# Performance work log

Hardware: AMD Instinct MI355X
Metric: run time of the kernel (lower is better)

The kernel has to match this reference:

```python
import math
import jax, jax.numpy as jnp
import numpy as np

NUM_HEAD = 8
EPS = 1e-5

def _ln(v, w, b):
    m = jnp.mean(v, axis=-1, keepdims=True)
    var = jnp.var(v, axis=-1, keepdims=True)  # biased var, as torch LayerNorm
    return (v - m) * jax.lax.rsqrt(var + EPS) * w + b

def setup_inputs() -> dict:
    key = jax.random.key(0)
    ks = jax.random.split(key, 5)
    B, T, D, L, Hd = 16, 2048, 512, 768, 512
    return {
        "x": jax.random.normal(ks[0], (B, T, D), jnp.float32),
        "xf": jax.random.normal(ks[1], (B, T, L), jnp.float32),
        "norm_w": jnp.ones((D,), jnp.float32),
        "norm_b": jnp.zeros((D,), jnp.float32),
        "tnorm_w": jnp.ones((L,), jnp.float32),
        "tnorm_b": jnp.zeros((L,), jnp.float32),
        "Wq": jax.random.normal(ks[2], (Hd, D), jnp.float32) * (1.0 / math.sqrt(D)),
        "Wk": jax.random.normal(ks[3], (Hd, L), jnp.float32) * (1.0 / math.sqrt(L)),
        "Wv": jax.random.normal(ks[4], (Hd, L), jnp.float32) * (1.0 / math.sqrt(L)),
    }

def reference(x, xf, norm_w, norm_b, tnorm_w, tnorm_b, Wq, Wk, Wv):
    B, T, _ = x.shape
    Hd = Wq.shape[0]
    H = NUM_HEAD
    d = Hd // H
    q = _ln(x, norm_w, norm_b) @ Wq.T                 # B,T,Hd
    xf_n = _ln(xf, tnorm_w, tnorm_b)
    k = xf_n @ Wk.T                                   # B,T,Hd (N == T)
    v = xf_n @ Wv.T                                   # B,T,Hd
    qh = q.reshape(B, T, H, d)
    kh = k.reshape(B, T, H, d)
    vh = v.reshape(B, T, H, d)
    # per-position, per-head dot product gate (no softmax)
    w = jnp.einsum('bthd,bthd->bth', qh, kh) / math.sqrt(d)
    # dropout in eval mode = identity
    y2 = (w[..., None] * vh).reshape(B, T, Hd)
    y1 = ((1.0 - w)[..., None] * qh).reshape(B, T, Hd)
    return (y1, y2)
```

## Files before the change

kernel.cpp:

```cpp
#include <hip/hip_runtime.h>

#define NT 512
#define MT 64

typedef __attribute__((ext_vector_type(8))) short short8;
typedef __attribute__((ext_vector_type(4))) float f32x4;
typedef __attribute__((ext_vector_type(4))) unsigned short u16x4;

__device__ __forceinline__ unsigned short f2bf(float f) {
  unsigned int u = __builtin_bit_cast(unsigned int, f);
  u += 0x7fffu + ((u >> 16) & 1u);
  return (unsigned short)(u >> 16);
}

__global__ void cvt_weights(const float* __restrict__ wq,
                            const float* __restrict__ wk,
                            const float* __restrict__ wv,
                            unsigned short* __restrict__ o) {
  int stride = gridDim.x * blockDim.x;
  int i0 = blockIdx.x * blockDim.x + threadIdx.x;
  for (int t = i0; t < 32768; t += stride) {
    int lane = t & 63, n = (t >> 6) & 3, kk32 = (t >> 8) & 15, head = t >> 12;
    int row = head * 64 + n * 16 + (lane & 15);
    int k   = kk32 * 32 + (lane >> 4) * 8;
    const float* s = wq + (size_t)row * 512 + k;
    unsigned short* d = o + (size_t)t * 8;
    #pragma unroll
    for (int e = 0; e < 8; ++e) d[e] = f2bf(s[e]);
  }
  for (int t = i0; t < 49152; t += stride) {
    int lane = t & 63, n = (t >> 6) & 3, rem = t >> 8;
    int kk32 = rem % 24, head = rem / 24;
    int row = head * 64 + n * 16 + (lane & 15);
    int k   = kk32 * 32 + (lane >> 4) * 8;
    const float* s = wk + (size_t)row * 768 + k;
    unsigned short* d = o + 262144 + (size_t)t * 8;
    #pragma unroll
    for (int e = 0; e < 8; ++e) d[e] = f2bf(s[e]);
  }
  for (int t = i0; t < 49152; t += stride) {
    int lane = t & 63, n = (t >> 6) & 3, rem = t >> 8;
    int kk32 = rem % 24, head = rem / 24;
    int row = head * 64 + n * 16 + (lane & 15);
    int k   = kk32 * 32 + (lane >> 4) * 8;
    const float* s = wv + (size_t)row * 768 + k;
    unsigned short* d = o + 655360 + (size_t)t * 8;
    #pragma unroll
    for (int e = 0; e < 8; ++e) d[e] = f2bf(s[e]);
  }
}

__global__ __launch_bounds__(NT, 2)
void fused_xattn(const float* __restrict__ x, const float* __restrict__ xf,
                 const float* __restrict__ nw, const float* __restrict__ nb,
                 const float* __restrict__ tw, const float* __restrict__ tb,
                 const unsigned short* __restrict__ wbf,
                 float* __restrict__ out) {
  __shared__ __attribute__((aligned(16))) char smem[98304];
  const int tid   = threadIdx.x;
  const int lane  = tid & 63;
  const int wid   = tid >> 6;
  const int lr    = lane & 15;
  const int lkb   = (lane >> 4) * 8;
  const int lrow4 = (lane >> 4) * 4;

  const long row0 = (long)blockIdx.x * MT;
  float* __restrict__ y1 = out;
  float* __restrict__ y2 = out + 16777216L;

  {
    f32x4 t0[8], t1[8];
    #pragma unroll
    for (int j = 0; j < 8; ++j) {
      const f32x4* rp = (const f32x4*)(x + (row0 + wid + 8 * j) * 512);
      t0[j] = rp[lane]; t1[j] = rp[lane + 64];
    }
    const f32x4* g4 = (const f32x4*)nw;
    const f32x4* b4 = (const f32x4*)nb;
    f32x4 g0 = g4[lane], g1 = g4[lane + 64];
    f32x4 c0 = b4[lane], c1 = b4[lane + 64];
    #pragma unroll
    for (int j = 0; j < 8; ++j) {
      f32x4 a = t0[j], b = t1[j];
      float s  = a.x + a.y + a.z + a.w + b.x + b.y + b.z + b.w;
      float s2 = a.x*a.x + a.y*a.y + a.z*a.z + a.w*a.w
               + b.x*b.x + b.y*b.y + b.z*b.z + b.w*b.w;
      #pragma unroll
      for (int m = 1; m < 64; m <<= 1) { s += __shfl_xor(s, m, 64); s2 += __shfl_xor(s2, m, 64); }
      float mean = s * (1.0f / 512.0f);
      float var  = s2 * (1.0f / 512.0f) - mean * mean;
      float rs   = rsqrtf(var + 1e-5f);
      u16x4 o0 = { f2bf((a.x - mean) * rs * g0.x + c0.x),
                   f2bf((a.y - mean) * rs * g0.y + c0.y),
                   f2bf((a.z - mean) * rs * g0.z + c0.z),
                   f2bf((a.w - mean) * rs * g0.w + c0.w) };
      u16x4 o1 = { f2bf((b.x - mean) * rs * g1.x + c1.x),
                   f2bf((b.y - mean) * rs * g1.y + c1.y),
                   f2bf((b.z - mean) * rs * g1.z + c1.z),
                   f2bf((b.w - mean) * rs * g1.w + c1.w) };
      int r = wid + 8 * j;
      int base = r * 1024, sw = (r & 7) << 4;
      *(u16x4*)(smem + ((base +       lane * 8) ^ sw)) = o0;
      *(u16x4*)(smem + ((base + 512 + lane * 8) ^ sw)) = o1;
    }
  }
  __syncthreads();

  f32x4 fr0[8], fr1[8], fr2[8];
  #pragma unroll
  for (int j = 0; j < 8; ++j) {
    const f32x4* rp = (const f32x4*)(xf + (row0 + wid + 8 * j) * 768);
    fr0[j] = rp[lane]; fr1[j] = rp[lane + 64]; fr2[j] = rp[lane + 128];
  }

  f32x4 qa[4][4] = {};
  {
    const unsigned short* bq = wbf + wid * 32768 + lane * 8;
    short8 bc[4], ac[4];
    #pragma unroll
    for (int n = 0; n < 4; ++n) bc[n] = *(const short8*)(bq + n * 512);
    #pragma unroll
    for (int m = 0; m < 4; ++m) {
      int row = m * 16 + lr;
      ac[m] = *(const short8*)(smem + ((row * 1024 + lkb * 2) ^ ((row & 7) << 4)));
    }
    for (int kk = 0; kk < 16; ++kk) {
      short8 bn[4], an[4];
      if (kk < 15) {
        #pragma unroll
        for (int n = 0; n < 4; ++n)
          bn[n] = *(const short8*)(bq + (kk + 1) * 2048 + n * 512);
        #pragma unroll
        for (int m = 0; m < 4; ++m) {
          int row = m * 16 + lr;
          an[m] = *(const short8*)(smem + ((row * 1024 + ((kk + 1) * 32 + lkb) * 2) ^ ((row & 7) << 4)));
        }
      }
      #pragma unroll
      for (int n = 0; n < 4; ++n)
        #pragma unroll
        for (int m = 0; m < 4; ++m)
          qa[m][n] = __builtin_amdgcn_mfma_f32_16x16x32_bf16(ac[m], bc[n], qa[m][n], 0, 0, 0);
      if (kk < 15) {
        #pragma unroll
        for (int n = 0; n < 4; ++n) bc[n] = bn[n];
        #pragma unroll
        for (int m = 0; m < 4; ++m) ac[m] = an[m];
      }
    }
  }
  __syncthreads();

  {
    const f32x4* g4 = (const f32x4*)tw;
    const f32x4* b4 = (const f32x4*)tb;
    f32x4 g0 = g4[lane], g1 = g4[lane + 64], g2 = g4[lane + 128];
    f32x4 c0 = b4[lane], c1 = b4[lane + 64], c2 = b4[lane + 128];
    #pragma unroll
    for (int j = 0; j < 8; ++j) {
      f32x4 a = fr0[j], b = fr1[j], c = fr2[j];
      float s  = a.x + a.y + a.z + a.w + b.x + b.y + b.z + b.w
               + c.x + c.y + c.z + c.w;
      float s2 = a.x*a.x + a.y*a.y + a.z*a.z + a.w*a.w
               + b.x*b.x + b.y*b.y + b.z*b.z + b.w*b.w
               + c.x*c.x + c.y*c.y + c.z*c.z + c.w*c.w;
      #pragma unroll
      for (int m = 1; m < 64; m <<= 1) { s += __shfl_xor(s, m, 64); s2 += __shfl_xor(s2, m, 64); }
      float mean = s * (1.0f / 768.0f);
      float var  = s2 * (1.0f / 768.0f) - mean * mean;
      float rs   = rsqrtf(var + 1e-5f);
      u16x4 o0 = { f2bf((a.x - mean) * rs * g0.x + c0.x),
                   f2bf((a.y - mean) * rs * g0.y + c0.y),
                   f2bf((a.z - mean) * rs * g0.z + c0.z),
                   f2bf((a.w - mean) * rs * g0.w + c0.w) };
      u16x4 o1 = { f2bf((b.x - mean) * rs * g1.x + c1.x),
                   f2bf((b.y - mean) * rs * g1.y + c1.y),
                   f2bf((b.z - mean) * rs * g1.z + c1.z),
                   f2bf((b.w - mean) * rs * g1.w + c1.w) };
      u16x4 o2 = { f2bf((c.x - mean) * rs * g2.x + c2.x),
                   f2bf((c.y - mean) * rs * g2.y + c2.y),
                   f2bf((c.z - mean) * rs * g2.z + c2.z),
                   f2bf((c.w - mean) * rs * g2.w + c2.w) };
      int r = wid + 8 * j;
      int base = r * 1536, sw = (r & 7) << 4;
      *(u16x4*)(smem + ((base +        lane * 8) ^ sw)) = o0;
      *(u16x4*)(smem + ((base + 512  + lane * 8) ^ sw)) = o1;
      *(u16x4*)(smem + ((base + 1024 + lane * 8) ^ sw)) = o2;
    }
  }
  __syncthreads();

  f32x4 ka[4][4] = {};
  {
    const unsigned short* bk = wbf + 262144 + wid * 49152 + lane * 8;
    short8 bc[4], ac[4];
    #pragma unroll
    for (int n = 0; n < 4; ++n) bc[n] = *(const short8*)(bk + n * 512);
    #pragma unroll
    for (int m = 0; m < 4; ++m) {
      int row = m * 16 + lr;
      ac[m] = *(const short8*)(smem + ((row * 1536 + lkb * 2) ^ ((row & 7) << 4)));
    }
    for (int kk = 0; kk < 24; ++kk) {
      short8 bn[4], an[4];
      if (kk < 23) {
        #pragma unroll
        for (int n = 0; n < 4; ++n)
          bn[n] = *(const short8*)(bk + (kk + 1) * 2048 + n * 512);
        #pragma unroll
        for (int m = 0; m < 4; ++m) {
          int row = m * 16 + lr;
          an[m] = *(const short8*)(smem + ((row * 1536 + ((kk + 1) * 32 + lkb) * 2) ^ ((row & 7) << 4)));
        }
      }
      #pragma unroll
      for (int n = 0; n < 4; ++n)
        #pragma unroll
        for (int m = 0; m < 4; ++m)
          ka[m][n] = __builtin_amdgcn_mfma_f32_16x16x32_bf16(ac[m], bc[n], ka[m][n], 0, 0, 0);
      if (kk < 23) {
        #pragma unroll
        for (int n = 0; n < 4; ++n) bc[n] = bn[n];
        #pragma unroll
        for (int m = 0; m < 4; ++m) ac[m] = an[m];
      }
    }
  }

  float wgt[4][4];
  #pragma unroll
  for (int m = 0; m < 4; ++m) {
    #pragma unroll
    for (int r = 0; r < 4; ++r) {
      float p = 0.0f;
      #pragma unroll
      for (int n = 0; n < 4; ++n) p += qa[m][n][r] * ka[m][n][r];
      #pragma unroll
      for (int msk = 1; msk < 16; msk <<= 1) p += __shfl_xor(p, msk, 64);
      wgt[m][r] = p * 0.125f;
    }
  }
  #pragma unroll
  for (int m = 0; m < 4; ++m) {
    #pragma unroll
    for (int r = 0; r < 4; ++r) {
      float f = 1.0f - wgt[m][r];
      long grow = row0 + m * 16 + lrow4 + r;
      #pragma unroll
      for (int n = 0; n < 4; ++n) {
        int ch = wid * 64 + n * 16 + lr;
        y1[grow * 512 + ch] = f * qa[m][n][r];
      }
    }
  }

  f32x4 va[4][4] = {};
  {
    const unsigned short* bv = wbf + 655360 + wid * 49152 + lane * 8;
    short8 bc[4], ac[4];
    #pragma unroll
    for (int n = 0; n < 4; ++n) bc[n] = *(const short8*)(bv + n * 512);
    #pragma unroll
    for (int m = 0; m < 4; ++m) {
      int row = m * 16 + lr;
      ac[m] = *(const short8*)(smem + ((row * 1536 + lkb * 2) ^ ((row & 7) << 4)));
    }
    for (int kk = 0; kk < 24; ++kk) {
      short8 bn[4], an[4];
      if (kk < 23) {
        #pragma unroll
        for (int n = 0; n < 4; ++n)
          bn[n] = *(const short8*)(bv + (kk + 1) * 2048 + n * 512);
        #pragma unroll
        for (int m = 0; m < 4; ++m) {
          int row = m * 16 + lr;
          an[m] = *(const short8*)(smem + ((row * 1536 + ((kk + 1) * 32 + lkb) * 2) ^ ((row & 7) << 4)));
        }
      }
      #pragma unroll
      for (int n = 0; n < 4; ++n)
        #pragma unroll
        for (int m = 0; m < 4; ++m)
          va[m][n] = __builtin_amdgcn_mfma_f32_16x16x32_bf16(ac[m], bc[n], va[m][n], 0, 0, 0);
      if (kk < 23) {
        #pragma unroll
        for (int n = 0; n < 4; ++n) bc[n] = bn[n];
        #pragma unroll
        for (int m = 0; m < 4; ++m) ac[m] = an[m];
      }
    }
  }
  #pragma unroll
  for (int m = 0; m < 4; ++m) {
    #pragma unroll
    for (int r = 0; r < 4; ++r) {
      float f = wgt[m][r];
      long grow = row0 + m * 16 + lrow4 + r;
      #pragma unroll
      for (int n = 0; n < 4; ++n) {
        int ch = wid * 64 + n * 16 + lr;
        y2[grow * 512 + ch] = f * va[m][n][r];
      }
    }
  }
}

extern "C" void kernel_launch(void* const* d_in, const int* in_sizes, int n_in,
                              void* d_out, int out_size, void* d_ws, size_t ws_size,
                              hipStream_t stream) {
  const float* x  = (const float*)d_in[0];
  const float* xf = (const float*)d_in[1];
  const float* nw = (const float*)d_in[2];
  const float* nb = (const float*)d_in[3];
  const float* tw = (const float*)d_in[4];
  const float* tb = (const float*)d_in[5];
  const float* wq = (const float*)d_in[6];
  const float* wk = (const float*)d_in[7];
  const float* wv = (const float*)d_in[8];
  unsigned short* wbf = (unsigned short*)d_ws;

  cvt_weights<<<256, 256, 0, stream>>>(wq, wk, wv, wbf);
  fused_xattn<<<512, NT, 0, stream>>>(x, xf, nw, nb, tw, tb, wbf, (float*)d_out);
}
```

Baseline: 117.2 us.

## Halve row tile, double grid, and reorder LN/GEMM stages with separate smem buffers

```diff
diff --git a/kernel.cpp b/kernel.cpp
--- a/kernel.cpp
+++ b/kernel.cpp
@@ -1,7 +1,7 @@
 #include <hip/hip_runtime.h>
 
 #define NT 512
-#define MT 64
+#define MT 32
 
 typedef __attribute__((ext_vector_type(8))) short short8;
 typedef __attribute__((ext_vector_type(4))) float f32x4;
@@ -50,13 +50,15 @@
   }
 }
 
-__global__ __launch_bounds__(NT, 2)
+__global__ __launch_bounds__(NT, 4)
 void fused_xattn(const float* __restrict__ x, const float* __restrict__ xf,
                  const float* __restrict__ nw, const float* __restrict__ nb,
                  const float* __restrict__ tw, const float* __restrict__ tb,
                  const unsigned short* __restrict__ wbf,
                  float* __restrict__ out) {
-  __shared__ __attribute__((aligned(16))) char smem[98304];
+  __shared__ __attribute__((aligned(16))) char smem[81920];
+  char* bufA = smem;
+  char* bufB = smem + 49152;
   const int tid   = threadIdx.x;
   const int lane  = tid & 63;
   const int wid   = tid >> 6;
@@ -69,96 +71,19 @@
   float* __restrict__ y2 = out + 16777216L;
 
   {
-    f32x4 t0[8], t1[8];
-    #pragma unroll
-    for (int j = 0; j < 8; ++j) {
-      const f32x4* rp = (const f32x4*)(x + (row0 + wid + 8 * j) * 512);
-      t0[j] = rp[lane]; t1[j] = rp[lane + 64];
-    }
-    const f32x4* g4 = (const f32x4*)nw;
-    const f32x4* b4 = (const f32x4*)nb;
-    f32x4 g0 = g4[lane], g1 = g4[lane + 64];
-    f32x4 c0 = b4[lane], c1 = b4[lane + 64];
-    #pragma unroll
-    for (int j = 0; j < 8; ++j) {
-      f32x4 a = t0[j], b = t1[j];
-      float s  = a.x + a.y + a.z + a.w + b.x + b.y + b.z + b.w;
-      float s2 = a.x*a.x + a.y*a.y + a.z*a.z + a.w*a.w
-               + b.x*b.x + b.y*b.y + b.z*b.z + b.w*b.w;
-      #pragma unroll
-      for (int m = 1; m < 64; m <<= 1) { s += __shfl_xor(s, m, 64); s2 += __shfl_xor(s2, m, 64); }
-      float mean = s * (1.0f / 512.0f);
-      float var  = s2 * (1.0f / 512.0f) - mean * mean;
-      float rs   = rsqrtf(var + 1e-5f);
-      u16x4 o0 = { f2bf((a.x - mean) * rs * g0.x + c0.x),
-                   f2bf((a.y - mean) * rs * g0.y + c0.y),
-                   f2bf((a.z - mean) * rs * g0.z + c0.z),
-                   f2bf((a.w - mean) * rs * g0.w + c0.w) };
-      u16x4 o1 = { f2bf((b.x - mean) * rs * g1.x + c1.x),
-                   f2bf((b.y - mean) * rs * g1.y + c1.y),
-                   f2bf((b.z - mean) * rs * g1.z + c1.z),
-                   f2bf((b.w - mean) * rs * g1.w + c1.w) };
-      int r = wid + 8 * j;
-      int base = r * 1024, sw = (r & 7) << 4;
-      *(u16x4*)(smem + ((base +       lane * 8) ^ sw)) = o0;
-      *(u16x4*)(smem + ((base + 512 + lane * 8) ^ sw)) = o1;
-    }
-  }
-  __syncthreads();
-
-  f32x4 fr0[8], fr1[8], fr2[8];
-  #pragma unroll
-  for (int j = 0; j < 8; ++j) {
-    const f32x4* rp = (const f32x4*)(xf + (row0 + wid + 8 * j) * 768);
-    fr0[j] = rp[lane]; fr1[j] = rp[lane + 64]; fr2[j] = rp[lane + 128];
-  }
-
-  f32x4 qa[4][4] = {};
-  {
-    const unsigned short* bq = wbf + wid * 32768 + lane * 8;
-    short8 bc[4], ac[4];
-    #pragma unroll
-    for (int n = 0; n < 4; ++n) bc[n] = *(const short8*)(bq + n * 512);
-    #pragma unroll
-    for (int m = 0; m < 4; ++m) {
-      int row = m * 16 + lr;
-      ac[m] = *(const short8*)(smem + ((row * 1024 + lkb * 2) ^ ((row & 7) << 4)));
-    }
-    for (int kk = 0; kk < 16; ++kk) {
-      short8 bn[4], an[4];
-      if (kk < 15) {
-        #pragma unroll
-        for (int n = 0; n < 4; ++n)
-          bn[n] = *(const short8*)(bq + (kk + 1) * 2048 + n * 512);
-        #pragma unroll
-        for (int m = 0; m < 4; ++m) {
-          int row = m * 16 + lr;
-          an[m] = *(const short8*)(smem + ((row * 1024 + ((kk + 1) * 32 + lkb) * 2) ^ ((row & 7) << 4)));
-        }
-      }
-      #pragma unroll
-      for (int n = 0; n < 4; ++n)
-        #pragma unroll
-        for (int m = 0; m < 4; ++m)
-          qa[m][n] = __builtin_amdgcn_mfma_f32_16x16x32_bf16(ac[m], bc[n], qa[m][n], 0, 0, 0);
-      if (kk < 15) {
-        #pragma unroll
-        for (int n = 0; n < 4; ++n) bc[n] = bn[n];
-        #pragma unroll
-        for (int m = 0; m < 4; ++m) ac[m] = an[m];
-      }
-    }
-  }
-  __syncthreads();
-
-  {
+    f32x4 t0[4], t1[4], t2[4];
+    #pragma unroll
+    for (int j = 0; j < 4; ++j) {
+      const f32x4* rp = (const f32x4*)(xf + (row0 + wid * 4 + j) * 768);
+      t0[j] = rp[lane]; t1[j] = rp[lane + 64]; t2[j] = rp[lane + 128];
+    }
     const f32x4* g4 = (const f32x4*)tw;
     const f32x4* b4 = (const f32x4*)tb;
     f32x4 g0 = g4[lane], g1 = g4[lane + 64], g2 = g4[lane + 128];
     f32x4 c0 = b4[lane], c1 = b4[lane + 64], c2 = b4[lane + 128];
     #pragma unroll
-    for (int j = 0; j < 8; ++j) {
-      f32x4 a = fr0[j], b = fr1[j], c = fr2[j];
+    for (int j = 0; j < 4; ++j) {
+      f32x4 a = t0[j], b = t1[j], c = t2[j];
       float s  = a.x + a.y + a.z + a.w + b.x + b.y + b.z + b.w
                + c.x + c.y + c.z + c.w;
       float s2 = a.x*a.x + a.y*a.y + a.z*a.z + a.w*a.w
@@ -181,55 +106,131 @@
                    f2bf((c.y - mean) * rs * g2.y + c2.y),
                    f2bf((c.z - mean) * rs * g2.z + c2.z),
                    f2bf((c.w - mean) * rs * g2.w + c2.w) };
-      int r = wid + 8 * j;
+      int r = wid * 4 + j;
       int base = r * 1536, sw = (r & 7) << 4;
-      *(u16x4*)(smem + ((base +        lane * 8) ^ sw)) = o0;
-      *(u16x4*)(smem + ((base + 512  + lane * 8) ^ sw)) = o1;
-      *(u16x4*)(smem + ((base + 1024 + lane * 8) ^ sw)) = o2;
-    }
+      *(u16x4*)(bufA + ((base +        lane * 8) ^ sw)) = o0;
+      *(u16x4*)(bufA + ((base + 512  + lane * 8) ^ sw)) = o1;
+      *(u16x4*)(bufA + ((base + 1024 + lane * 8) ^ sw)) = o2;
+    }
+  }
+
+  f32x4 xr0[4], xr1[4];
+  #pragma unroll
+  for (int j = 0; j < 4; ++j) {
+    const f32x4* rp = (const f32x4*)(x + (row0 + wid * 4 + j) * 512);
+    xr0[j] = rp[lane]; xr1[j] = rp[lane + 64];
   }
   __syncthreads();
 
-  f32x4 ka[4][4] = {};
+  f32x4 ka[2][4] = {};
   {
     const unsigned short* bk = wbf + 262144 + wid * 49152 + lane * 8;
-    short8 bc[4], ac[4];
+    short8 bc[4], ac[2];
     #pragma unroll
     for (int n = 0; n < 4; ++n) bc[n] = *(const short8*)(bk + n * 512);
     #pragma unroll
-    for (int m = 0; m < 4; ++m) {
+    for (int m = 0; m < 2; ++m) {
       int row = m * 16 + lr;
-      ac[m] = *(const short8*)(smem + ((row * 1536 + lkb * 2) ^ ((row & 7) << 4)));
+      ac[m] = *(const short8*)(bufA + ((row * 1536 + lkb * 2) ^ ((row & 7) << 4)));
     }
     for (int kk = 0; kk < 24; ++kk) {
-      short8 bn[4], an[4];
+      short8 bn[4], an[2];
       if (kk < 23) {
         #pragma unroll
         for (int n = 0; n < 4; ++n)
           bn[n] = *(const short8*)(bk + (kk + 1) * 2048 + n * 512);
         #pragma unroll
-        for (int m = 0; m < 4; ++m) {
+        for (int m = 0; m < 2; ++m) {
           int row = m * 16 + lr;
-          an[m] = *(const short8*)(smem + ((row * 1536 + ((kk + 1) * 32 + lkb) * 2) ^ ((row & 7) << 4)));
+          an[m] = *(const short8*)(bufA + ((row * 1536 + ((kk + 1) * 32 + lkb) * 2) ^ ((row & 7) << 4)));
         }
       }
       #pragma unroll
       for (int n = 0; n < 4; ++n)
         #pragma unroll
-        for (int m = 0; m < 4; ++m)
+        for (int m = 0; m < 2; ++m)
           ka[m][n] = __builtin_amdgcn_mfma_f32_16x16x32_bf16(ac[m], bc[n], ka[m][n], 0, 0, 0);
       if (kk < 23) {
         #pragma unroll
         for (int n = 0; n < 4; ++n) bc[n] = bn[n];
         #pragma unroll
-        for (int m = 0; m < 4; ++m) ac[m] = an[m];
-      }
-    }
-  }
-
-  float wgt[4][4];
+        for (int m = 0; m < 2; ++m) ac[m] = an[m];
+      }
+    }
+  }
+
+  {
+    const f32x4* g4 = (const f32x4*)nw;
+    const f32x4* b4 = (const f32x4*)nb;
+    f32x4 g0 = g4[lane], g1 = g4[lane + 64];
+    f32x4 c0 = b4[lane], c1 = b4[lane + 64];
+    #pragma unroll
+    for (int j = 0; j < 4; ++j) {
+      f32x4 a = xr0[j], b = xr1[j];
+      float s  = a.x + a.y + a.z + a.w + b.x + b.y + b.z + b.w;
+      float s2 = a.x*a.x + a.y*a.y + a.z*a.z + a.w*a.w
+               + b.x*b.x + b.y*b.y + b.z*b.z + b.w*b.w;
+      #pragma unroll
+      for (int m = 1; m < 64; m <<= 1) { s += __shfl_xor(s, m, 64); s2 += __shfl_xor(s2, m, 64); }
+      float mean = s * (1.0f / 512.0f);
+      float var  = s2 * (1.0f / 512.0f) - mean * mean;
+      float rs   = rsqrtf(var + 1e-5f);
+      u16x4 o0 = { f2bf((a.x - mean) * rs * g0.x + c0.x),
+                   f2bf((a.y - mean) * rs * g0.y + c0.y),
+                   f2bf((a.z - mean) * rs * g0.z + c0.z),
+                   f2bf((a.w - mean) * rs * g0.w + c0.w) };
+      u16x4 o1 = { f2bf((b.x - mean) * rs * g1.x + c1.x),
+                   f2bf((b.y - mean) * rs * g1.y + c1.y),
+                   f2bf((b.z - mean) * rs * g1.z + c1.z),
+                   f2bf((b.w - mean) * rs * g1.w + c1.w) };
+      int r = wid * 4 + j;
+      int base = r * 1024, sw = (r & 7) << 4;
+      *(u16x4*)(bufB + ((base +       lane * 8) ^ sw)) = o0;
+      *(u16x4*)(bufB + ((base + 512 + lane * 8) ^ sw)) = o1;
+    }
+  }
+  __syncthreads();
+
+  f32x4 qa[2][4] = {};
+  {
+    const unsigned short* bq = wbf + wid * 32768 + lane * 8;
+    short8 bc[4], ac[2];
+    #pragma unroll
+    for (int n = 0; n < 4; ++n) bc[n] = *(const short8*)(bq + n * 512);
+    #pragma unroll
+    for (int m = 0; m < 2; ++m) {
+      int row = m * 16 + lr;
+      ac[m] = *(const short8*)(bufB + ((row * 1024 + lkb * 2) ^ ((row & 7) << 4)));
+    }
+    for (int kk = 0; kk < 16; ++kk) {
+      short8 bn[4], an[2];
+      if (kk < 15) {
+        #pragma unroll
+        for (int n = 0; n < 4; ++n)
+          bn[n] = *(const short8*)(bq + (kk + 1) * 2048 + n * 512);
+        #pragma unroll
+        for (int m = 0; m < 2; ++m) {
+          int row = m * 16 + lr;
+          an[m] = *(const short8*)(bufB + ((row * 1024 + ((kk + 1) * 32 + lkb) * 2) ^ ((row & 7) << 4)));
+        }
+      }
+      #pragma unroll
+      for (int n = 0; n < 4; ++n)
+        #pragma unroll
+        for (int m = 0; m < 2; ++m)
+          qa[m][n] = __builtin_amdgcn_mfma_f32_16x16x32_bf16(ac[m], bc[n], qa[m][n], 0, 0, 0);
+      if (kk < 15) {
+        #pragma unroll
+        for (int n = 0; n < 4; ++n) bc[n] = bn[n];
+        #pragma unroll
+        for (int m = 0; m < 2; ++m) ac[m] = an[m];
+      }
+    }
+  }
+
+  float wgt[2][4];
   #pragma unroll
-  for (int m = 0; m < 4; ++m) {
+  for (int m = 0; m < 2; ++m) {
     #pragma unroll
     for (int r = 0; r < 4; ++r) {
       float p = 0.0f;
@@ -241,7 +242,7 @@
     }
   }
   #pragma unroll
-  for (int m = 0; m < 4; ++m) {
+  for (int m = 0; m < 2; ++m) {
     #pragma unroll
     for (int r = 0; r < 4; ++r) {
       float f = 1.0f - wgt[m][r];
@@ -254,44 +255,44 @@
     }
   }
 
-  f32x4 va[4][4] = {};
+  f32x4 va[2][4] = {};
   {
     const unsigned short* bv = wbf + 655360 + wid * 49152 + lane * 8;
-    short8 bc[4], ac[4];
+    short8 bc[4], ac[2];
     #pragma unroll
     for (int n = 0; n < 4; ++n) bc[n] = *(const short8*)(bv + n * 512);
     #pragma unroll
-    for (int m = 0; m < 4; ++m) {
+    for (int m = 0; m < 2; ++m) {
       int row = m * 16 + lr;
-      ac[m] = *(const short8*)(smem + ((row * 1536 + lkb * 2) ^ ((row & 7) << 4)));
+      ac[m] = *(const short8*)(bufA + ((row * 1536 + lkb * 2) ^ ((row & 7) << 4)));
     }
     for (int kk = 0; kk < 24; ++kk) {
-      short8 bn[4], an[4];
+      short8 bn[4], an[2];
       if (kk < 23) {
         #pragma unroll
         for (int n = 0; n < 4; ++n)
           bn[n] = *(const short8*)(bv + (kk + 1) * 2048 + n * 512);
         #pragma unroll
-        for (int m = 0; m < 4; ++m) {
+        for (int m = 0; m < 2; ++m) {
           int row = m * 16 + lr;
-          an[m] = *(const short8*)(smem + ((row * 1536 + ((kk + 1) * 32 + lkb) * 2) ^ ((row & 7) << 4)));
+          an[m] = *(const short8*)(bufA + ((row * 1536 + ((kk + 1) * 32 + lkb) * 2) ^ ((row & 7) << 4)));
         }
       }
       #pragma unroll
       for (int n = 0; n < 4; ++n)
         #pragma unroll
-        for (int m = 0; m < 4; ++m)
+        for (int m = 0; m < 2; ++m)
           va[m][n] = __builtin_amdgcn_mfma_f32_16x16x32_bf16(ac[m], bc[n], va[m][n], 0, 0, 0);
       if (kk < 23) {
         #pragma unroll
         for (int n = 0; n < 4; ++n) bc[n] = bn[n];
         #pragma unroll
-        for (int m = 0; m < 4; ++m) ac[m] = an[m];
+        for (int m = 0; m < 2; ++m) ac[m] = an[m];
       }
     }
   }
   #pragma unroll
-  for (int m = 0; m < 4; ++m) {
+  for (int m = 0; m < 2; ++m) {
     #pragma unroll
     for (int r = 0; r < 4; ++r) {
       float f = wgt[m][r];
@@ -320,5 +321,5 @@
   unsigned short* wbf = (unsigned short*)d_ws;
 
   cvt_weights<<<256, 256, 0, stream>>>(wq, wk, wv, wbf);
-  fused_xattn<<<512, NT, 0, stream>>>(x, xf, nw, nb, tw, tb, wbf, (float*)d_out);
+  fused_xattn<<<1024, NT, 0, stream>>>(x, xf, nw, nb, tw, tb, wbf, (float*)d_out);
 }
```

After: 196.3 us. 67.4% more time.

## Process two row tiles per block and prefetch next xf tile during GEMMs

Applied to the files above, without the earlier changes.

```diff
diff --git a/kernel.cpp b/kernel.cpp
--- a/kernel.cpp
+++ b/kernel.cpp
@@ -1,7 +1,6 @@
 #include <hip/hip_runtime.h>
 
 #define NT 512
-#define MT 64
 
 typedef __attribute__((ext_vector_type(8))) short short8;
 typedef __attribute__((ext_vector_type(4))) float f32x4;
@@ -56,7 +55,8 @@
                  const float* __restrict__ tw, const float* __restrict__ tb,
                  const unsigned short* __restrict__ wbf,
                  float* __restrict__ out) {
-  __shared__ __attribute__((aligned(16))) char smem[98304];
+  __shared__ __attribute__((aligned(16))) char ldsF[98304];
+  __shared__ __attribute__((aligned(16))) char ldsX[65536];
   const int tid   = threadIdx.x;
   const int lane  = tid & 63;
   const int wid   = tid >> 6;
@@ -64,244 +64,271 @@
   const int lkb   = (lane >> 4) * 8;
   const int lrow4 = (lane >> 4) * 4;
 
-  const long row0 = (long)blockIdx.x * MT;
   float* __restrict__ y1 = out;
   float* __restrict__ y2 = out + 16777216L;
 
+  f32x4 fr0[8], fr1[8], fr2[8];
   {
-    f32x4 t0[8], t1[8];
+    const long r0 = (long)blockIdx.x * 128;
+    #pragma unroll
+    for (int j = 0; j < 8; ++j) {
+      const f32x4* rp = (const f32x4*)(xf + (r0 + wid + 8 * j) * 768);
+      fr0[j] = rp[lane]; fr1[j] = rp[lane + 64]; fr2[j] = rp[lane + 128];
+    }
+  }
+
+  #pragma unroll
+  for (int t = 0; t < 2; ++t) {
+    const long row0 = (long)blockIdx.x * 128 + t * 64;
+
+    {
+      const f32x4* g4 = (const f32x4*)tw;
+      const f32x4* b4 = (const f32x4*)tb;
+      f32x4 g0 = g4[lane], g1 = g4[lane + 64], g2 = g4[lane + 128];
+      f32x4 c0 = b4[lane], c1 = b4[lane + 64], c2 = b4[lane + 128];
+      #pragma unroll
+      for (int j = 0; j < 8; ++j) {
+        f32x4 a = fr0[j], b = fr1[j], c = fr2[j];
+        float s  = a.x + a.y + a.z + a.w + b.x + b.y + b.z + b.w
+                 + c.x + c.y + c.z + c.w;
+        float s2 = a.x*a.x + a.y*a.y + a.z*a.z + a.w*a.w
+                 + b.x*b.x + b.y*b.y + b.z*b.z + b.w*b.w
+                 + c.x*c.x + c.y*c.y + c.z*c.z + c.w*c.w;
+        #pragma unroll
+        for (int m = 1; m < 64; m <<= 1) { s += __shfl_xor(s, m, 64); s2 += __shfl_xor(s2, m, 64); }
+        float mean = s * (1.0f / 768.0f);
+        float var  = s2 * (1.0f / 768.0f) - mean * mean;
+        float rs   = rsqrtf(var + 1e-5f);
+        u16x4 o0 = { f2bf((a.x - mean) * rs * g0.x + c0.x),
+                     f2bf((a.y - mean) * rs * g0.y + c0.y),
+                     f2bf((a.z - mean) * rs * g0.z + c0.z),
+                     f2bf((a.w - mean) * rs * g0.w + c0.w) };
+        u16x4 o1 = { f2bf((b.x - mean) * rs * g1.x + c1.x),
+                     f2bf((b.y - mean) * rs * g1.y + c1.y),
+                     f2bf((b.z - mean) * rs * g1.z + c1.z),
+                     f2bf((b.w - mean) * rs * g1.w + c1.w) };
+        u16x4 o2 = { f2bf((c.x - mean) * rs * g2.x + c2.x),
+                     f2bf((c.y - mean) * rs * g2.y + c2.y),
+                     f2bf((c.z - mean) * rs * g2.z + c2.z),
+                     f2bf((c.w - mean) * rs * g2.w + c2.w) };
+        int r = wid + 8 * j;
+        int base = r * 1536, sw = (r & 7) << 4;
+        *(u16x4*)(ldsF + ((base +        lane * 8) ^ sw)) = o0;
+        *(u16x4*)(ldsF + ((base + 512  + lane * 8) ^ sw)) = o1;
+        *(u16x4*)(ldsF + ((base + 1024 + lane * 8) ^ sw)) = o2;
+      }
+    }
+    __syncthreads();
+
+    f32x4 xr0[8], xr1[8];
     #pragma unroll
     for (int j = 0; j < 8; ++j) {
       const f32x4* rp = (const f32x4*)(x + (row0 + wid + 8 * j) * 512);
-      t0[j] = rp[lane]; t1[j] = rp[lane + 64];
-    }
-    const f32x4* g4 = (const f32x4*)nw;
-    const f32x4* b4 = (const f32x4*)nb;
-    f32x4 g0 = g4[lane], g1 = g4[lane + 64];
-    f32x4 c0 = b4[lane], c1 = b4[lane + 64];
-    #pragma unroll
-    for (int j = 0; j < 8; ++j) {
-      f32x4 a = t0[j], b = t1[j];
-      float s  = a.x + a.y + a.z + a.w + b.x + b.y + b.z + b.w;
-      float s2 = a.x*a.x + a.y*a.y + a.z*a.z + a.w*a.w
-               + b.x*b.x + b.y*b.y + b.z*b.z + b.w*b.w;
-      #pragma unroll
-      for (int m = 1; m < 64; m <<= 1) { s += __shfl_xor(s, m, 64); s2 += __shfl_xor(s2, m, 64); }
-      float mean = s * (1.0f / 512.0f);
-      float var  = s2 * (1.0f / 512.0f) - mean * mean;
-      float rs   = rsqrtf(var + 1e-5f);
-      u16x4 o0 = { f2bf((a.x - mean) * rs * g0.x + c0.x),
-                   f2bf((a.y - mean) * rs * g0.y + c0.y),
-                   f2bf((a.z - mean) * rs * g0.z + c0.z),
-                   f2bf((a.w - mean) * rs * g0.w + c0.w) };
-      u16x4 o1 = { f2bf((b.x - mean) * rs * g1.x + c1.x),
-                   f2bf((b.y - mean) * rs * g1.y + c1.y),
-                   f2bf((b.z - mean) * rs * g1.z + c1.z),
-                   f2bf((b.w - mean) * rs * g1.w + c1.w) };
-      int r = wid + 8 * j;
-      int base = r * 1024, sw = (r & 7) << 4;
-      *(u16x4*)(smem + ((base +       lane * 8) ^ sw)) = o0;
-      *(u16x4*)(smem + ((base + 512 + lane * 8) ^ sw)) = o1;
-    }
-  }
-  __syncthreads();
-
-  f32x4 fr0[8], fr1[8], fr2[8];
-  #pragma unroll
-  for (int j = 0; j < 8; ++j) {
-    const f32x4* rp = (const f32x4*)(xf + (row0 + wid + 8 * j) * 768);
-    fr0[j] = rp[lane]; fr1[j] = rp[lane + 64]; fr2[j] = rp[lane + 128];
-  }
-
-  f32x4 qa[4][4] = {};
-  {
-    const unsigned short* bq = wbf + wid * 32768 + lane * 8;
-    short8 bc[4], ac[4];
-    #pragma unroll
-    for (int n = 0; n < 4; ++n) bc[n] = *(const short8*)(bq + n * 512);
+      xr0[j] = rp[lane]; xr1[j] = rp[lane + 64];
+    }
+
+    f32x4 ka[4][4] = {};
+    {
+      const unsigned short* bk = wbf + 262144 + wid * 49152 + lane * 8;
+      short8 bc[4], ac[4];
+      #pragma unroll
+      for (int n = 0; n < 4; ++n) bc[n] = *(const short8*)(bk + n * 512);
+      #pragma unroll
+      for (int m = 0; m < 4; ++m) {
+        int row = m * 16 + lr;
+        ac[m] = *(const short8*)(ldsF + ((row * 1536 + lkb * 2) ^ ((row & 7) << 4)));
+      }
+      for (int kk = 0; kk < 24; ++kk) {
+        short8 bn[4], an[4];
+        if (kk < 23) {
+          #pragma unroll
+          for (int n = 0; n < 4; ++n)
+            bn[n] = *(const short8*)(bk + (kk + 1) * 2048 + n * 512);
+          #pragma unroll
+          for (int m = 0; m < 4; ++m) {
+            int row = m * 16 + lr;
+            an[m] = *(const short8*)(ldsF + ((row * 1536 + ((kk + 1) * 32 + lkb) * 2) ^ ((row & 7) << 4)));
+          }
+        }
+        #pragma unroll
+        for (int n = 0; n < 4; ++n)
+          #pragma unroll
+          for (int m = 0; m < 4; ++m)
+            ka[m][n] = __builtin_amdgcn_mfma_f32_16x16x32_bf16(ac[m], bc[n], ka[m][n], 0, 0, 0);
+        if (kk < 23) {
+          #pragma unroll
+          for (int n = 0; n < 4; ++n) bc[n] = bn[n];
+          #pragma unroll
+          for (int m = 0; m < 4; ++m) ac[m] = an[m];
+        }
+      }
+    }
+
+    {
+      const f32x4* g4 = (const f32x4*)nw;
+      const f32x4* b4 = (const f32x4*)nb;
+      f32x4 g0 = g4[lane], g1 = g4[lane + 64];
+      f32x4 c0 = b4[lane], c1 = b4[lane + 64];
+      #pragma unroll
+      for (int j = 0; j < 8; ++j) {
+        f32x4 a = xr0[j], b = xr1[j];
+        float s  = a.x + a.y + a.z + a.w + b.x + b.y + b.z + b.w;
+        float s2 = a.x*a.x + a.y*a.y + a.z*a.z + a.w*a.w
+                 + b.x*b.x + b.y*b.y + b.z*b.z + b.w*b.w;
+        #pragma unroll
+        for (int m = 1; m < 64; m <<= 1) { s += __shfl_xor(s, m, 64); s2 += __shfl_xor(s2, m, 64); }
+        float mean = s * (1.0f / 512.0f);
+        float var  = s2 * (1.0f / 512.0f) - mean * mean;
+        float rs   = rsqrtf(var + 1e-5f);
+        u16x4 o0 = { f2bf((a.x - mean) * rs * g0.x + c0.x),
+                     f2bf((a.y - mean) * rs * g0.y + c0.y),
+                     f2bf((a.z - mean) * rs * g0.z + c0.z),
+                     f2bf((a.w - mean) * rs * g0.w + c0.w) };
+        u16x4 o1 = { f2bf((b.x - mean) * rs * g1.x + c1.x),
+                     f2bf((b.y - mean) * rs * g1.y + c1.y),
+                     f2bf((b.z - mean) * rs * g1.z + c1.z),
+                     f2bf((b.w - mean) * rs * g1.w + c1.w) };
+        int r = wid + 8 * j;
+        int base = r * 1024, sw = (r & 7) << 4;
+        *(u16x4*)(ldsX + ((base +       lane * 8) ^ sw)) = o0;
+        *(u16x4*)(ldsX + ((base + 512 + lane * 8) ^ sw)) = o1;
+      }
+    }
+    __syncthreads();
+
+    f32x4 qa[4][4] = {};
+    {
+      const unsigned short* bq = wbf + wid * 32768 + lane * 8;
+      short8 bc[4], ac[4];
+      #pragma unroll
+      for (int n = 0; n < 4; ++n) bc[n] = *(const short8*)(bq + n * 512);
+      #pragma unroll
+      for (int m = 0; m < 4; ++m) {
+        int row = m * 16 + lr;
+        ac[m] = *(const short8*)(ldsX + ((row * 1024 + lkb * 2) ^ ((row & 7) << 4)));
+      }
+      for (int kk = 0; kk < 16; ++kk) {
+        short8 bn[4], an[4];
+        if (kk < 15) {
+          #pragma unroll
+          for (int n = 0; n < 4; ++n)
+            bn[n] = *(const short8*)(bq + (kk + 1) * 2048 + n * 512);
+          #pragma unroll
+          for (int m = 0; m < 4; ++m) {
+            int row = m * 16 + lr;
+            an[m] = *(const short8*)(ldsX + ((row * 1024 + ((kk + 1) * 32 + lkb) * 2) ^ ((row & 7) << 4)));
+          }
+        }
+        #pragma unroll
+        for (int n = 0; n < 4; ++n)
+          #pragma unroll
+          for (int m = 0; m < 4; ++m)
+            qa[m][n] = __builtin_amdgcn_mfma_f32_16x16x32_bf16(ac[m], bc[n], qa[m][n], 0, 0, 0);
+        if (kk < 15) {
+          #pragma unroll
+          for (int n = 0; n < 4; ++n) bc[n] = bn[n];
+          #pragma unroll
+          for (int m = 0; m < 4; ++m) ac[m] = an[m];
+        }
+      }
+    }
+
+    float wgt[4][4];
     #pragma unroll
     for (int m = 0; m < 4; ++m) {
-      int row = m * 16 + lr;
-      ac[m] = *(const short8*)(smem + ((row * 1024 + lkb * 2) ^ ((row & 7) << 4)));
-    }
-    for (int kk = 0; kk < 16; ++kk) {
-      short8 bn[4], an[4];
-      if (kk < 15) {
+      #pragma unroll
+      for (int r = 0; r < 4; ++r) {
+        float p = 0.0f;
+        #pragma unroll
+        for (int n = 0; n < 4; ++n) p += qa[m][n][r] * ka[m][n][r];
+        #pragma unroll
+        for (int msk = 1; msk < 16; msk <<= 1) p += __shfl_xor(p, msk, 64);
+        wgt[m][r] = p * 0.125f;
+      }
+    }
+    #pragma unroll
+    for (int m = 0; m < 4; ++m) {
+      #pragma unroll
+      for (int r = 0; r < 4; ++r) {
+        float f = 1.0f - wgt[m][r];
+        long grow = row0 + m * 16 + lrow4 + r;
+        #pragma unroll
+        for (int n = 0; n < 4; ++n) {
+          int ch = wid * 64 + n * 16 + lr;
+          y1[grow * 512 + ch] = f * qa[m][n][r];
+        }
+      }
+    }
+
+    if (t == 0) {
+      const long r1 = (long)blockIdx.x * 128 + 64;
+      #pragma unroll
+      for (int j = 0; j < 6; ++j) {
+        const f32x4* rp = (const f32x4*)(xf + (r1 + wid + 8 * j) * 768);
+        fr0[j] = rp[lane]; fr1[j] = rp[lane + 64]; fr2[j] = rp[lane + 128];
+      }
+    }
+
+    f32x4 va[4][4] = {};
+    {
+      const unsigned short* bv = wbf + 655360 + wid * 49152 + lane * 8;
+      short8 bc[4], ac[4];
+      #pragma unroll
+      for (int n = 0; n < 4; ++n) bc[n] = *(const short8*)(bv + n * 512);
+      #pragma unroll
+      for (int m = 0; m < 4; ++m) {
+        int row = m * 16 + lr;
+        ac[m] = *(const short8*)(ldsF + ((row * 1536 + lkb * 2) ^ ((row & 7) << 4)));
+      }
+      for (int kk = 0; kk < 24; ++kk) {
+        short8 bn[4], an[4];
+        if (kk < 23) {
+          #pragma unroll
+          for (int n = 0; n < 4; ++n)
+            bn[n] = *(const short8*)(bv + (kk + 1) * 2048 + n * 512);
+          #pragma unroll
+          for (int m = 0; m < 4; ++m) {
+            int row = m * 16 + lr;
+            an[m] = *(const short8*)(ldsF + ((row * 1536 + ((kk + 1) * 32 + lkb) * 2) ^ ((row & 7) << 4)));
+          }
+        }
         #pragma unroll
         for (int n = 0; n < 4; ++n)
-          bn[n] = *(const short8*)(bq + (kk + 1) * 2048 + n * 512);
-        #pragma unroll
-        for (int m = 0; m < 4; ++m) {
-          int row = m * 16 + lr;
-          an[m] = *(const short8*)(smem + ((row * 1024 + ((kk + 1) * 32 + lkb) * 2) ^ ((row & 7) << 4)));
-        }
-      }
-      #pragma unroll
-      for (int n = 0; n < 4; ++n)
-        #pragma unroll
-        for (int m = 0; m < 4; ++m)
-          qa[m][n] = __builtin_amdgcn_mfma_f32_16x16x32_bf16(ac[m], bc[n], qa[m][n], 0, 0, 0);
-      if (kk < 15) {
-        #pragma unroll
-        for (int n = 0; n < 4; ++n) bc[n] = bn[n];
-        #pragma unroll
-        for (int m = 0; m < 4; ++m) ac[m] = an[m];
-      }
-    }
-  }
-  __syncthreads();
-
-  {
-    const f32x4* g4 = (const f32x4*)tw;
-    const f32x4* b4 = (const f32x4*)tb;
-    f32x4 g0 = g4[lane], g1 = g4[lane + 64], g2 = g4[lane + 128];
-    f32x4 c0 = b4[lane], c1 = b4[lane + 64], c2 = b4[lane + 128];
-    #pragma unroll
-    for (int j = 0; j < 8; ++j) {
-      f32x4 a = fr0[j], b = fr1[j], c = fr2[j];
-      float s  = a.x + a.y + a.z + a.w + b.x + b.y + b.z + b.w
-               + c.x + c.y + c.z + c.w;
-      float s2 = a.x*a.x + a.y*a.y + a.z*a.z + a.w*a.w
-               + b.x*b.x + b.y*b.y + b.z*b.z + b.w*b.w
-               + c.x*c.x + c.y*c.y + c.z*c.z + c.w*c.w;
-      #pragma unroll
-      for (int m = 1; m < 64; m <<= 1) { s += __shfl_xor(s, m, 64); s2 += __shfl_xor(s2, m, 64); }
-      float mean = s * (1.0f / 768.0f);
-      float var  = s2 * (1.0f / 768.0f) - mean * mean;
-      float rs   = rsqrtf(var + 1e-5f);
-      u16x4 o0 = { f2bf((a.x - mean) * rs * g0.x + c0.x),
-                   f2bf((a.y - mean) * rs * g0.y + c0.y),
-                   f2bf((a.z - mean) * rs * g0.z + c0.z),
-                   f2bf((a.w - mean) * rs * g0.w + c0.w) };
-      u16x4 o1 = { f2bf((b.x - mean) * rs * g1.x + c1.x),
-                   f2bf((b.y - mean) * rs * g1.y + c1.y),
-                   f2bf((b.z - mean) * rs * g1.z + c1.z),
-                   f2bf((b.w - mean) * rs * g1.w + c1.w) };
-      u16x4 o2 = { f2bf((c.x - mean) * rs * g2.x + c2.x),
-                   f2bf((c.y - mean) * rs * g2.y + c2.y),
-                   f2bf((c.z - mean) * rs * g2.z + c2.z),
-                   f2bf((c.w - mean) * rs * g2.w + c2.w) };
-      int r = wid + 8 * j;
-      int base = r * 1536, sw = (r & 7) << 4;
-      *(u16x4*)(smem + ((base +        lane * 8) ^ sw)) = o0;
-      *(u16x4*)(smem + ((base + 512  + lane * 8) ^ sw)) = o1;
-      *(u16x4*)(smem + ((base + 1024 + lane * 8) ^ sw)) = o2;
-    }
-  }
-  __syncthreads();
-
-  f32x4 ka[4][4] = {};
-  {
-    const unsigned short* bk = wbf + 262144 + wid * 49152 + lane * 8;
-    short8 bc[4], ac[4];
-    #pragma unroll
-    for (int n = 0; n < 4; ++n) bc[n] = *(const short8*)(bk + n * 512);
+          #pragma unroll
+          for (int m = 0; m < 4; ++m)
+            va[m][n] = __builtin_amdgcn_mfma_f32_16x16x32_bf16(ac[m], bc[n], va[m][n], 0, 0, 0);
+        if (kk < 23) {
+          #pragma unroll
+          for (int n = 0; n < 4; ++n) bc[n] = bn[n];
+          #pragma unroll
+          for (int m = 0; m < 4; ++m) ac[m] = an[m];
+        }
+      }
+    }
+
+    if (t == 0) {
+      const long r1 = (long)blockIdx.x * 128 + 64;
+      #pragma unroll
+      for (int j = 6; j < 8; ++j) {
+        const f32x4* rp = (const f32x4*)(xf + (r1 + wid + 8 * j) * 768);
+        fr0[j] = rp[lane]; fr1[j] = rp[lane + 64]; fr2[j] = rp[lane + 128];
+      }
+    }
+
     #pragma unroll
     for (int m = 0; m < 4; ++m) {
-      int row = m * 16 + lr;
-      ac[m] = *(const short8*)(smem + ((row * 1536 + lkb * 2) ^ ((row & 7) << 4)));
-    }
-    for (int kk = 0; kk < 24; ++kk) {
-      short8 bn[4], an[4];
-      if (kk < 23) {
-        #pragma unroll
-        for (int n = 0; n < 4; ++n)
-          bn[n] = *(const short8*)(bk + (kk + 1) * 2048 + n * 512);
-        #pragma unroll
-        for (int m = 0; m < 4; ++m) {
-          int row = m * 16 + lr;
-          an[m] = *(const short8*)(smem + ((row * 1536 + ((kk + 1) * 32 + lkb) * 2) ^ ((row & 7) << 4)));
-        }
-      }
-      #pragma unroll
-      for (int n = 0; n < 4; ++n)
-        #pragma unroll
-        for (int m = 0; m < 4; ++m)
-          ka[m][n] = __builtin_amdgcn_mfma_f32_16x16x32_bf16(ac[m], bc[n], ka[m][n], 0, 0, 0);
-      if (kk < 23) {
-        #pragma unroll
-        for (int n = 0; n < 4; ++n) bc[n] = bn[n];
-        #pragma unroll
-        for (int m = 0; m < 4; ++m) ac[m] = an[m];
-      }
-    }
-  }
-
-  float wgt[4][4];
-  #pragma unroll
-  for (int m = 0; m < 4; ++m) {
-    #pragma unroll
-    for (int r = 0; r < 4; ++r) {
-      float p = 0.0f;
-      #pragma unroll
-      for (int n = 0; n < 4; ++n) p += qa[m][n][r] * ka[m][n][r];
-      #pragma unroll
-      for (int msk = 1; msk < 16; msk <<= 1) p += __shfl_xor(p, msk, 64);
-      wgt[m][r] = p * 0.125f;
-    }
-  }
-  #pragma unroll
-  for (int m = 0; m < 4; ++m) {
-    #pragma unroll
-    for (int r = 0; r < 4; ++r) {
-      float f = 1.0f - wgt[m][r];
-      long grow = row0 + m * 16 + lrow4 + r;
-      #pragma unroll
-      for (int n = 0; n < 4; ++n) {
-        int ch = wid * 64 + n * 16 + lr;
-        y1[grow * 512 + ch] = f * qa[m][n][r];
-      }
-    }
-  }
-
-  f32x4 va[4][4] = {};
-  {
-    const unsigned short* bv = wbf + 655360 + wid * 49152 + lane * 8;
-    short8 bc[4], ac[4];
-    #pragma unroll
-    for (int n = 0; n < 4; ++n) bc[n] = *(const short8*)(bv + n * 512);
-    #pragma unroll
-    for (int m = 0; m < 4; ++m) {
-      int row = m * 16 + lr;
-      ac[m] = *(const short8*)(smem + ((row * 1536 + lkb * 2) ^ ((row & 7) << 4)));
-    }
-    for (int kk = 0; kk < 24; ++kk) {
-      short8 bn[4], an[4];
-      if (kk < 23) {
-        #pragma unroll
-        for (int n = 0; n < 4; ++n)
-          bn[n] = *(const short8*)(bv + (kk + 1) * 2048 + n * 512);
-        #pragma unroll
-        for (int m = 0; m < 4; ++m) {
-          int row = m * 16 + lr;
-          an[m] = *(const short8*)(smem + ((row * 1536 + ((kk + 1) * 32 + lkb) * 2) ^ ((row & 7) << 4)));
-        }
-      }
-      #pragma unroll
-      for (int n = 0; n < 4; ++n)
-        #pragma unroll
-        for (int m = 0; m < 4; ++m)
-          va[m][n] = __builtin_amdgcn_mfma_f32_16x16x32_bf16(ac[m], bc[n], va[m][n], 0, 0, 0);
-      if (kk < 23) {
-        #pragma unroll
-        for (int n = 0; n < 4; ++n) bc[n] = bn[n];
-        #pragma unroll
-        for (int m = 0; m < 4; ++m) ac[m] = an[m];
-      }
-    }
-  }
-  #pragma unroll
-  for (int m = 0; m < 4; ++m) {
-    #pragma unroll
-    for (int r = 0; r < 4; ++r) {
-      float f = wgt[m][r];
-      long grow = row0 + m * 16 + lrow4 + r;
-      #pragma unroll
-      for (int n = 0; n < 4; ++n) {
-        int ch = wid * 64 + n * 16 + lr;
-        y2[grow * 512 + ch] = f * va[m][n][r];
-      }
-    }
+      #pragma unroll
+      for (int r = 0; r < 4; ++r) {
+        float f = wgt[m][r];
+        long grow = row0 + m * 16 + lrow4 + r;
+        #pragma unroll
+        for (int n = 0; n < 4; ++n) {
+          int ch = wid * 64 + n * 16 + lr;
+          y2[grow * 512 + ch] = f * va[m][n][r];
+        }
+      }
+    }
+    __syncthreads();
   }
 }
 
@@ -320,5 +347,5 @@
   unsigned short* wbf = (unsigned short*)d_ws;
 
   cvt_weights<<<256, 256, 0, stream>>>(wq, wk, wv, wbf);
-  fused_xattn<<<512, NT, 0, stream>>>(x, xf, nw, nb, tw, tb, wbf, (float*)d_out);
+  fused_xattn<<<256, NT, 0, stream>>>(x, xf, nw, nb, tw, tb, wbf, (float*)d_out);
 }
```

New measurement: 235.0 us. 2x slower.
